# Kernel optimization log

Measured on AMD Instinct MI355X. Metric: run time of the kernel, lower is better.

Reference implementation:

```python
import jax, jax.numpy as jnp
import numpy as np

B, C, S = 128, 32, 512          # batch, input_channel, seq_len (= d_model of the encoders)
EMB = 256                       # embed_size
NHEAD = 8                       # args.num_heads (also TransformerEncoderLayer nhead)
DFF = 2048                      # torch TransformerEncoderLayer default dim_feedforward
RLEN = S // 2 + 1               # 257 rfft bins
HK = int(RLEN * 0.5)            # 128, 'hight_freq_k' split point
LK = RLEN - HK                  # 129

def _ln(x, w, b, axes=-1):
    m = jnp.mean(x, axis=axes, keepdims=True)
    v = jnp.var(x, axis=axes, keepdims=True)
    return (x - m) / jnp.sqrt(v + 1e-5) * w + b

def _tel(x, in_w, in_b, out_w, out_b, ln1w, ln1b, w1, b1, w2, b2, ln2w, ln2b):
    # torch nn.TransformerEncoderLayer (batch_first, post-norm, relu, eval-mode dropout)
    b_, s_, d_ = x.shape
    dh = d_ // NHEAD
    qkv = x @ in_w.T + in_b
    q, k, v = jnp.split(qkv, 3, axis=-1)
    sp = lambda t: t.reshape(b_, s_, NHEAD, dh).transpose(0, 2, 1, 3)
    q, k, v = sp(q), sp(k), sp(v)
    sc = jnp.einsum('bhqd,bhkd->bhqk', q, k) / jnp.sqrt(jnp.asarray(dh, x.dtype))
    att = jax.nn.softmax(sc, axis=-1)
    o = jnp.einsum('bhqk,bhkd->bhqd', att, v).transpose(0, 2, 1, 3).reshape(b_, s_, d_)
    o = o @ out_w.T + out_b
    x = _ln(x + o, ln1w, ln1b)
    f = jax.nn.relu(x @ w1.T + b1) @ w2.T + b2
    return _ln(x + f, ln2w, ln2b)

def _crelu(z):
    return jax.lax.complex(jax.nn.relu(z.real), jax.nn.relu(z.imag))

def _csoftmax(z):
    return jax.lax.complex(jax.nn.softmax(z.real, axis=-1), jax.nn.softmax(z.imag, axis=-1))

def _cattn(q):
    # self-attention with complex Q=K=V (no conjugate, per torch matmul(Q, K^T))
    dk = q.shape[-1]
    sc = jnp.einsum('bqe,bke->bqk', q, q) / jnp.asarray(dk, jnp.float32) ** 0.5
    return jnp.einsum('bqk,bke->bqe', _csoftmax(sc), q)

def setup_inputs() -> dict:
    key = jax.random.key(0)
    ks = iter(jax.random.split(key, 64))
    n = lambda *sh: jax.random.normal(next(ks), sh, jnp.float32) * 0.02
    d = {'x': jax.random.normal(next(ks), (B, C, S), jnp.float32)}
    for p in ('t', 'r'):
        d[p + '_in_w'] = n(3 * S, S);  d[p + '_in_b'] = jnp.zeros((3 * S,), jnp.float32)
        d[p + '_out_w'] = n(S, S);     d[p + '_out_b'] = jnp.zeros((S,), jnp.float32)
        d[p + '_ln1_w'] = jnp.ones((S,), jnp.float32); d[p + '_ln1_b'] = jnp.zeros((S,), jnp.float32)
        d[p + '_lin1_w'] = n(DFF, S); d[p + '_lin1_b'] = jnp.zeros((DFF,), jnp.float32)
        d[p + '_lin2_w'] = n(S, DFF); d[p + '_lin2_b'] = jnp.zeros((S,), jnp.float32)
        d[p + '_ln2_w'] = jnp.ones((S,), jnp.float32); d[p + '_ln2_b'] = jnp.zeros((S,), jnp.float32)
    d['lc_w'] = n(S, S);  d['lc_b'] = jnp.zeros((S,), jnp.float32)
    d['up1_w'] = n(S, S); d['up1_b'] = jnp.zeros((S,), jnp.float32)
    d['up2_w'] = n(S, S); d['up2_b'] = jnp.zeros((S,), jnp.float32)
    d['n1_w'] = jnp.ones((C, S), jnp.float32); d['n1_b'] = jnp.zeros((C, S), jnp.float32)
    d['n2_w'] = jnp.ones((C, S), jnp.float32); d['n2_b'] = jnp.zeros((C, S), jnp.float32)
    d['l1_re'] = jax.random.normal(next(ks), (HK, EMB), jnp.float32)
    d['l1_im'] = jax.random.normal(next(ks), (HK, EMB), jnp.float32)
    d['h1_re'] = jax.random.normal(next(ks), (LK, EMB), jnp.float32)
    d['h1_im'] = jax.random.normal(next(ks), (LK, EMB), jnp.float32)
    d['lb1_re'] = jax.random.normal(next(ks), (EMB,), jnp.float32)
    d['lb1_im'] = jax.random.normal(next(ks), (EMB,), jnp.float32)
    d['hb1_re'] = jax.random.normal(next(ks), (EMB,), jnp.float32)
    d['hb1_im'] = jax.random.normal(next(ks), (EMB,), jnp.float32)
    return d

def reference(x, t_in_w, t_in_b, t_out_w, t_out_b, t_ln1_w, t_ln1_b, t_lin1_w, t_lin1_b, t_lin2_w, t_lin2_b, t_ln2_w, t_ln2_b, r_in_w, r_in_b, r_out_w, r_out_b, r_ln1_w, r_ln1_b, r_lin1_w, r_lin1_b, r_lin2_w, r_lin2_b, r_ln2_w, r_ln2_b, lc_w, lc_b, up1_w, up1_b, up2_w, up2_b, n1_w, n1_b, n2_w, n2_b, l1_re, l1_im, h1_re, h1_im, lb1_re, lb1_im, hb1_re, hb1_im):
    l1 = jax.lax.complex(l1_re, l1_im)
    h1 = jax.lax.complex(h1_re, h1_im)
    lb1 = jax.lax.complex(lb1_re, lb1_im)
    hb1 = jax.lax.complex(hb1_re, hb1_im)
    down_x = x  # downsample_scale=1 and padding_length=0 -> identity (i=0 path)
    # main branch
    df = jax.nn.relu(_tel(down_x, t_in_w, t_in_b, t_out_w, t_out_b, t_ln1_w, t_ln1_b,
                          t_lin1_w, t_lin1_b, t_lin2_w, t_lin2_b, t_ln2_w, t_ln2_b))
    df = _ln(df, n1_w, n1_b, axes=(-2, -1))
    # ttf_freqaug
    xf = jnp.fft.rfft(down_x, norm='ortho')                      # [B, C, 257] complex
    low = _crelu(jnp.einsum('bdk,ke->bde', xf[..., :HK], l1) + lb1)
    high = _crelu(jnp.einsum('bdk,ke->bde', xf[..., HK:], h1) + hb1)
    low = low + _cattn(low)
    high = high + _cattn(high)
    xcat = jnp.concatenate([low, high[..., low.shape[-1]:]], axis=-1)  # EMB bins (high slice is empty)
    fa = jnp.fft.irfft(xcat, n=S, norm='ortho')                  # zero-pads 256 -> 257 bins
    fa = fa @ lc_w.T + lc_b                                      # linear_change
    up = (fa @ up1_w.T + up1_b) @ up2_w.T + up2_b                # linear_up_sampling
    # recons branch
    rf = jax.nn.relu(_tel(fa, r_in_w, r_in_b, r_out_w, r_out_b, r_ln1_w, r_ln1_b,
                          r_lin1_w, r_lin1_b, r_lin2_w, r_lin2_b, r_ln2_w, r_ln2_b))
    rf = _ln(rf, n2_w, n2_b, axes=(-2, -1))
    res = df + rf
    return (res, down_x, fa, up)
```

## Files before the change

kernel.cpp:

```cpp
#include <hip/hip_runtime.h>
#include <math.h>


#define NROW 4096
#define NOUT 2097152

typedef __attribute__((ext_vector_type(8))) short short8;
typedef __attribute__((ext_vector_type(4))) float floatx4;

__device__ __forceinline__ unsigned short f2bf(float f) {
    union { float f; unsigned u; } v; v.f = f;
    return (unsigned short)((v.u + 0x7fffu + ((v.u >> 16) & 1u)) >> 16);
}
__device__ __forceinline__ float bf2f(unsigned short h) {
    union { unsigned u; float f; } v; v.u = ((unsigned)h) << 16;
    return v.f;
}

__device__ __forceinline__ void gload16(const unsigned short* g, unsigned short* l) {
    __builtin_amdgcn_global_load_lds((const __attribute__((address_space(1))) void*)g,
                                     (__attribute__((address_space(3))) void*)l, 16, 0, 0);
}

__device__ __forceinline__ void xcd_swizzle(int& bx, int& by, int& bz) {
    const int gx = gridDim.x, gy = gridDim.y;
    const int nwg = gx * gy * gridDim.z;
    int b = (bz * gy + by) * gx + bx;
    const int chunk = nwg >> 3;
    const int lb = (b & 7) * chunk + (b >> 3);
    bx = lb % gx;
    const int rem = lb / gx;
    by = rem % gy;
    bz = rem / gy;
}

__global__ __launch_bounds__(256) void tab_kernel(float* __restrict__ tabC, float* __restrict__ tabS)
{
    int n = blockIdx.x, k = threadIdx.x;
    int m = (n * k) & 511;
    float th = (float)m * 0.01227184630308513f;
    float s, c; sincosf(th, &s, &c);
    tabC[n * 256 + k] = c;
    tabS[n * 256 + k] = s;
}

__global__ __launch_bounds__(256) void wawm_kernel(const float* __restrict__ l1_re, const float* __restrict__ l1_im,
                                                   const float* __restrict__ lc_w,
                                                   const float* __restrict__ tabC, const float* __restrict__ tabS,
                                                   unsigned short* __restrict__ WaH, unsigned short* __restrict__ WaL,
                                                   unsigned short* __restrict__ WmH, unsigned short* __restrict__ WmL)
{
    __shared__ float lw[512];
    const float inv = 0.04419417382415922f;
    if (blockIdx.z == 0) {
        int n  = blockIdx.x;
        int ep = blockIdx.y * 256 + threadIdx.x;
        float acc = 0.f;
        if (ep < 256) {
            for (int k = 0; k < 128; ++k) {
                float c = tabC[n * 256 + k], s = tabS[n * 256 + k];
                acc += c * l1_re[k * 256 + ep] + s * l1_im[k * 256 + ep];
            }
        } else {
            int e = ep - 256;
            for (int k = 0; k < 128; ++k) {
                float c = tabC[n * 256 + k], s = tabS[n * 256 + k];
                acc += c * l1_im[k * 256 + e] - s * l1_re[k * 256 + e];
            }
        }
        float v = acc * inv;
        size_t idx = (size_t)ep * 512 + n;
        unsigned short h = f2bf(v);
        WaH[idx] = h;
        WaL[idx] = f2bf(v - bf2f(h));
    } else {
        int s  = blockIdx.x;
        int kk = blockIdx.y * 256 + threadIdx.x;
        for (int i = threadIdx.x; i < 512; i += 256) lw[i] = lc_w[s * 512 + i];
        __syncthreads();
        float acc = 0.f;
        if (kk < 256) {
            int k = kk;
            for (int n = 0; n < 512; ++n) acc += tabC[n * 256 + k] * lw[n];
            acc *= (k == 0) ? inv : 2.f * inv;
        } else {
            int k = kk - 256;
            if (k == 0) acc = 0.f;
            else {
                for (int n = 0; n < 512; ++n) acc += tabS[n * 256 + k] * lw[n];
                acc *= -2.f * inv;
            }
        }
        size_t idx = (size_t)s * 512 + kk;
        unsigned short h = f2bf(acc);
        WmH[idx] = h;
        WmL[idx] = f2bf(acc - bf2f(h));
    }
}

__global__ __launch_bounds__(256) void uber_prep_kernel(
    const float* s0, const float* s1, const float* s2, const float* s3, const float* s4,
    const float* s5, const float* s6, const float* s7, const float* s8, const float* s9,
    unsigned short* __restrict__ o, unsigned short* __restrict__ rinLo,
    const float* __restrict__ x, unsigned short* __restrict__ xhi,
    unsigned short* __restrict__ xlo, float* __restrict__ xcp,
    const float* __restrict__ lbre, const float* __restrict__ lbim, float* __restrict__ lbout)
{
    const int bid = blockIdx.x, tid = threadIdx.x;
    if (bid < 26624) {
        int i = bid * 256 + tid;
        const float* s; int off;
        if (i < 3145728) {
            if (i < 1048576) { if (i < 786432) { s = s0; off = 0; } else { s = s1; off = 786432; } }
            else             { if (i < 2097152) { s = s2; off = 1048576; } else { s = s3; off = 2097152; } }
        } else {
            if (i < 5242880) {
                if (i < 3932160) { s = s4; off = 3145728; }
                else if (i < 4194304) { s = s5; off = 3932160; }
                else { s = s6; off = 4194304; }
            } else {
                if (i < 6291456) { s = s7; off = 5242880; }
                else if (i < 6553600) { s = s8; off = 6291456; }
                else { s = s9; off = 6553600; }
            }
        }
        float v = s[i - off];
        unsigned short h = f2bf(v);
        o[i] = h;
        if (i >= 3145728 && i < 3932160) rinLo[i - 3145728] = f2bf(v - bf2f(h));
    } else if (bid < 34816) {
        int i = (bid - 26624) * 256 + tid;
        float v = x[i];
        unsigned short h = f2bf(v);
        xhi[i] = h;
        xlo[i] = f2bf(v - bf2f(h));
        xcp[i] = v;
    } else {
        int i = (bid - 34816) * 256 + tid;
        if (i < 512) lbout[i] = (i < 256) ? lbre[i] : lbim[i - 256];
    }
}

template <int TM, int TN, int ACT, int WF, int WBF>
__global__ __launch_bounds__(256) void gemm_mfma(
    const unsigned short* __restrict__ A, const unsigned short* __restrict__ W,
    const float* __restrict__ bias, float* __restrict__ Cf,
    unsigned short* __restrict__ Cb, int N, int K)
{
    constexpr int MI = TM / 32, NJ = TN / 32;
    constexpr int ARW = TM / 4, BRW = TN / 4;
    __shared__ unsigned short As[2][TM * 32];
    __shared__ unsigned short Bs[2][TN * 32];
    const int tid = threadIdx.x;
    const int wave = tid >> 6, lane = tid & 63;
    int bx = blockIdx.x, by = blockIdx.y, bz = blockIdx.z;
    xcd_swizzle(bx, by, bz);
    const int m0 = by * TM, n0 = bx * TN;
    const int sr = lane >> 2, sc = (lane & 3) * 8;
    const unsigned short* aS = A + (size_t)(m0 + wave * ARW + sr) * K + sc;
    const unsigned short* wS = W + (size_t)(n0 + wave * BRW + sr) * K + sc;
    const int wm = (wave >> 1) * (TM / 2), wn = (wave & 1) * (TN / 2);
    const int fr = lane & 15, fko = (lane >> 4) * 8;

    floatx4 acc[MI][NJ];
#pragma unroll
    for (int i = 0; i < MI; ++i)
#pragma unroll
        for (int j = 0; j < NJ; ++j) acc[i][j] = (floatx4){0.f, 0.f, 0.f, 0.f};

    for (int k0 = 0; k0 < K; k0 += 64) {
#pragma unroll
        for (int h = 0; h < 2; ++h) {
#pragma unroll
            for (int c = 0; c < ARW / 16; ++c)
                gload16(aS + (size_t)(16 * c) * K + k0 + 32 * h, &As[h][(wave * ARW + 16 * c) * 32]);
#pragma unroll
            for (int c = 0; c < BRW / 16; ++c)
                gload16(wS + (size_t)(16 * c) * K + k0 + 32 * h, &Bs[h][(wave * BRW + 16 * c) * 32]);
        }
        __syncthreads();
#pragma unroll
        for (int h = 0; h < 2; ++h) {
            short8 af[MI], bfr[NJ];
#pragma unroll
            for (int i = 0; i < MI; ++i) af[i] = *(const short8*)&As[h][(wm + i * 16 + fr) * 32 + fko];
#pragma unroll
            for (int j = 0; j < NJ; ++j) bfr[j] = *(const short8*)&Bs[h][(wn + j * 16 + fr) * 32 + fko];
#pragma unroll
            for (int i = 0; i < MI; ++i)
#pragma unroll
                for (int j = 0; j < NJ; ++j)
                    acc[i][j] = __builtin_amdgcn_mfma_f32_16x16x32_bf16(af[i], bfr[j], acc[i][j], 0, 0, 0);
        }
        __syncthreads();
    }
    const int r0 = m0 + wm + (lane >> 4) * 4;
#pragma unroll
    for (int i = 0; i < MI; ++i) {
#pragma unroll
        for (int j = 0; j < NJ; ++j) {
            int n = n0 + wn + j * 16 + fr;
            float bv = bias[n];
#pragma unroll
            for (int r = 0; r < 4; ++r) {
                int m = r0 + i * 16 + r;
                size_t idx = (size_t)m * N + n;
                float v = acc[i][j][r] + bv;
                if (ACT) v = fmaxf(v, 0.f);
                if (WF) Cf[idx] = v;
                if (WBF) Cb[idx] = f2bf(v);
            }
        }
    }
}

template <int TM, int TN, int ACT, int WBF>
__global__ __launch_bounds__(256) void gemm_dual(
    const unsigned short* __restrict__ A0, const unsigned short* __restrict__ A1,
    const unsigned short* __restrict__ W0, const unsigned short* __restrict__ W1,
    const float* __restrict__ b0, const float* __restrict__ b1,
    float* __restrict__ C0, float* __restrict__ C1,
    unsigned short* __restrict__ D0, unsigned short* __restrict__ D1, int N, int K)
{
    constexpr int MI = TM / 32, NJ = TN / 32;
    constexpr int ARW = TM / 4, BRW = TN / 4;
    __shared__ unsigned short As[2][TM * 32];
    __shared__ unsigned short Bs[2][TN * 32];
    const int tid = threadIdx.x;
    const int wave = tid >> 6, lane = tid & 63;
    int bx = blockIdx.x, by = blockIdx.y, bz = blockIdx.z;
    xcd_swizzle(bx, by, bz);
    const int m0 = by * TM, n0 = bx * TN;
    const int z = bz;
    const unsigned short* A = z ? A1 : A0;
    const unsigned short* W = z ? W1 : W0;
    const float* bias = z ? b1 : b0;
    float* Cf = z ? C1 : C0;
    unsigned short* Cb = z ? D1 : D0;
    const int sr = lane >> 2, sc = (lane & 3) * 8;
    const unsigned short* aS = A + (size_t)(m0 + wave * ARW + sr) * K + sc;
    const unsigned short* wS = W + (size_t)(n0 + wave * BRW + sr) * K + sc;
    const int wm = (wave >> 1) * (TM / 2), wn = (wave & 1) * (TN / 2);
    const int fr = lane & 15, fko = (lane >> 4) * 8;

    floatx4 acc[MI][NJ];
#pragma unroll
    for (int i = 0; i < MI; ++i)
#pragma unroll
        for (int j = 0; j < NJ; ++j) acc[i][j] = (floatx4){0.f, 0.f, 0.f, 0.f};

    for (int k0 = 0; k0 < K; k0 += 64) {
#pragma unroll
        for (int h = 0; h < 2; ++h) {
#pragma unroll
            for (int c = 0; c < ARW / 16; ++c)
                gload16(aS + (size_t)(16 * c) * K + k0 + 32 * h, &As[h][(wave * ARW + 16 * c) * 32]);
#pragma unroll
            for (int c = 0; c < BRW / 16; ++c)
                gload16(wS + (size_t)(16 * c) * K + k0 + 32 * h, &Bs[h][(wave * BRW + 16 * c) * 32]);
        }
        __syncthreads();
#pragma unroll
        for (int h = 0; h < 2; ++h) {
            short8 af[MI], bfr[NJ];
#pragma unroll
            for (int i = 0; i < MI; ++i) af[i] = *(const short8*)&As[h][(wm + i * 16 + fr) * 32 + fko];
#pragma unroll
            for (int j = 0; j < NJ; ++j) bfr[j] = *(const short8*)&Bs[h][(wn + j * 16 + fr) * 32 + fko];
#pragma unroll
            for (int i = 0; i < MI; ++i)
#pragma unroll
                for (int j = 0; j < NJ; ++j)
                    acc[i][j] = __builtin_amdgcn_mfma_f32_16x16x32_bf16(af[i], bfr[j], acc[i][j], 0, 0, 0);
        }
        __syncthreads();
    }
    const int r0 = m0 + wm + (lane >> 4) * 4;
#pragma unroll
    for (int i = 0; i < MI; ++i) {
#pragma unroll
        for (int j = 0; j < NJ; ++j) {
            int n = n0 + wn + j * 16 + fr;
            float bv = bias[n];
#pragma unroll
            for (int r = 0; r < 4; ++r) {
                int m = r0 + i * 16 + r;
                size_t idx = (size_t)m * N + n;
                float v = acc[i][j][r] + bv;
                if (ACT) v = fmaxf(v, 0.f);
                if (WBF) Cb[idx] = f2bf(v);
                else     Cf[idx] = v;
            }
        }
    }
}

template <int TM, int TN, int ACT, int WCOPY, int WHILO>
__global__ __launch_bounds__(256) void gemm_mfma3(
    const unsigned short* __restrict__ Ah, const unsigned short* __restrict__ Al,
    const unsigned short* __restrict__ Wh, const unsigned short* __restrict__ Wl,
    const float* __restrict__ bias, float* __restrict__ Cf, float* __restrict__ Ccopy,
    unsigned short* __restrict__ Hh, unsigned short* __restrict__ Hl, int N, int K)
{
    constexpr int MI = TM / 32, NJ = TN / 32;
    constexpr int ARW = TM / 4, BRW = TN / 4;
    __shared__ unsigned short Ash[2][TM * 32];
    __shared__ unsigned short Asl[2][TM * 32];
    __shared__ unsigned short Bsh[2][TN * 32];
    __shared__ unsigned short Bsl[2][TN * 32];
    const int tid = threadIdx.x;
    const int wave = tid >> 6, lane = tid & 63;
    int bx = blockIdx.x, by = blockIdx.y, bz = blockIdx.z;
    xcd_swizzle(bx, by, bz);
    const int m0 = by * TM, n0 = bx * TN;
    const int sr = lane >> 2, sc = (lane & 3) * 8;
    const size_t aoff = (size_t)(m0 + wave * ARW + sr) * K + sc;
    const size_t woff = (size_t)(n0 + wave * BRW + sr) * K + sc;
    const int wm = (wave >> 1) * (TM / 2), wn = (wave & 1) * (TN / 2);
    const int fr = lane & 15, fko = (lane >> 4) * 8;

    floatx4 acc[MI][NJ];
#pragma unroll
    for (int i = 0; i < MI; ++i)
#pragma unroll
        for (int j = 0; j < NJ; ++j) acc[i][j] = (floatx4){0.f, 0.f, 0.f, 0.f};

    for (int k0 = 0; k0 < K; k0 += 64) {
#pragma unroll
        for (int h = 0; h < 2; ++h) {
#pragma unroll
            for (int c = 0; c < ARW / 16; ++c) {
                gload16(Ah + aoff + (size_t)(16 * c) * K + k0 + 32 * h, &Ash[h][(wave * ARW + 16 * c) * 32]);
                gload16(Al + aoff + (size_t)(16 * c) * K + k0 + 32 * h, &Asl[h][(wave * ARW + 16 * c) * 32]);
            }
#pragma unroll
            for (int c = 0; c < BRW / 16; ++c) {
                gload16(Wh + woff + (size_t)(16 * c) * K + k0 + 32 * h, &Bsh[h][(wave * BRW + 16 * c) * 32]);
                gload16(Wl + woff + (size_t)(16 * c) * K + k0 + 32 * h, &Bsl[h][(wave * BRW + 16 * c) * 32]);
            }
        }
        __syncthreads();
#pragma unroll
        for (int h = 0; h < 2; ++h) {
            short8 ah[MI], al[MI], bh[NJ], bl[NJ];
#pragma unroll
            for (int i = 0; i < MI; ++i) {
                ah[i] = *(const short8*)&Ash[h][(wm + i * 16 + fr) * 32 + fko];
                al[i] = *(const short8*)&Asl[h][(wm + i * 16 + fr) * 32 + fko];
            }
#pragma unroll
            for (int j = 0; j < NJ; ++j) {
                bh[j] = *(const short8*)&Bsh[h][(wn + j * 16 + fr) * 32 + fko];
                bl[j] = *(const short8*)&Bsl[h][(wn + j * 16 + fr) * 32 + fko];
            }
#pragma unroll
            for (int i = 0; i < MI; ++i)
#pragma unroll
                for (int j = 0; j < NJ; ++j) {
                    acc[i][j] = __builtin_amdgcn_mfma_f32_16x16x32_bf16(al[i], bh[j], acc[i][j], 0, 0, 0);
                    acc[i][j] = __builtin_amdgcn_mfma_f32_16x16x32_bf16(ah[i], bl[j], acc[i][j], 0, 0, 0);
                    acc[i][j] = __builtin_amdgcn_mfma_f32_16x16x32_bf16(ah[i], bh[j], acc[i][j], 0, 0, 0);
                }
        }
        __syncthreads();
    }
    const int r0 = m0 + wm + (lane >> 4) * 4;
#pragma unroll
    for (int i = 0; i < MI; ++i) {
#pragma unroll
        for (int j = 0; j < NJ; ++j) {
            int n = n0 + wn + j * 16 + fr;
            float bv = bias[n];
#pragma unroll
            for (int r = 0; r < 4; ++r) {
                int m = r0 + i * 16 + r;
                size_t idx = (size_t)m * N + n;
                float v = acc[i][j][r] + bv;
                if (ACT) v = fmaxf(v, 0.f);
                Cf[idx] = v;
                if (WCOPY) Ccopy[idx] = v;
                if (WHILO) {
                    unsigned short h = f2bf(v);
                    Hh[idx] = h;
                    Hl[idx] = f2bf(v - bf2f(h));
                }
            }
        }
    }
}

template <int TM, int TN>
__global__ __launch_bounds__(256) void gemm_qkv_dual(
    const unsigned short* __restrict__ Ah0, const unsigned short* __restrict__ Al0,
    const unsigned short* __restrict__ Wh0, const unsigned short* __restrict__ Wl0,
    const float* __restrict__ b0, float* __restrict__ C0,
    const unsigned short* __restrict__ A1, const unsigned short* __restrict__ W1,
    const float* __restrict__ b1, unsigned short* __restrict__ C1,
    int N, int K)
{
    constexpr int MI = TM / 32, NJ = TN / 32;
    constexpr int ARW = TM / 4, BRW = TN / 4;
    __shared__ unsigned short Ash[2][TM * 32];
    __shared__ unsigned short Asl[2][TM * 32];
    __shared__ unsigned short Bsh[2][TN * 32];
    __shared__ unsigned short Bsl[2][TN * 32];
    const int tid = threadIdx.x;
    const int wave = tid >> 6, lane = tid & 63;
    int bx = blockIdx.x, by = blockIdx.y, bz = blockIdx.z;
    xcd_swizzle(bx, by, bz);
    const int m0 = by * TM, n0 = bx * TN;
    const int sr = lane >> 2, sc = (lane & 3) * 8;
    const size_t aoff = (size_t)(m0 + wave * ARW + sr) * K + sc;
    const size_t woff = (size_t)(n0 + wave * BRW + sr) * K + sc;
    const int wm = (wave >> 1) * (TM / 2), wn = (wave & 1) * (TN / 2);
    const int fr = lane & 15, fko = (lane >> 4) * 8;

    floatx4 acc[MI][NJ];
#pragma unroll
    for (int i = 0; i < MI; ++i)
#pragma unroll
        for (int j = 0; j < NJ; ++j) acc[i][j] = (floatx4){0.f, 0.f, 0.f, 0.f};

    const int r0 = m0 + wm + (lane >> 4) * 4;

    if (bz == 0) {
        for (int k0 = 0; k0 < K; k0 += 64) {
#pragma unroll
            for (int h = 0; h < 2; ++h) {
#pragma unroll
                for (int c = 0; c < ARW / 16; ++c) {
                    gload16(Ah0 + aoff + (size_t)(16 * c) * K + k0 + 32 * h, &Ash[h][(wave * ARW + 16 * c) * 32]);
                    gload16(Al0 + aoff + (size_t)(16 * c) * K + k0 + 32 * h, &Asl[h][(wave * ARW + 16 * c) * 32]);
                }
#pragma unroll
                for (int c = 0; c < BRW / 16; ++c) {
                    gload16(Wh0 + woff + (size_t)(16 * c) * K + k0 + 32 * h, &Bsh[h][(wave * BRW + 16 * c) * 32]);
                    gload16(Wl0 + woff + (size_t)(16 * c) * K + k0 + 32 * h, &Bsl[h][(wave * BRW + 16 * c) * 32]);
                }
            }
            __syncthreads();
#pragma unroll
            for (int h = 0; h < 2; ++h) {
                short8 ah[MI], al[MI], bh[NJ], bl[NJ];
#pragma unroll
                for (int i = 0; i < MI; ++i) {
                    ah[i] = *(const short8*)&Ash[h][(wm + i * 16 + fr) * 32 + fko];
                    al[i] = *(const short8*)&Asl[h][(wm + i * 16 + fr) * 32 + fko];
                }
#pragma unroll
                for (int j = 0; j < NJ; ++j) {
                    bh[j] = *(const short8*)&Bsh[h][(wn + j * 16 + fr) * 32 + fko];
                    bl[j] = *(const short8*)&Bsl[h][(wn + j * 16 + fr) * 32 + fko];
                }
#pragma unroll
                for (int i = 0; i < MI; ++i)
#pragma unroll
                    for (int j = 0; j < NJ; ++j) {
                        acc[i][j] = __builtin_amdgcn_mfma_f32_16x16x32_bf16(al[i], bh[j], acc[i][j], 0, 0, 0);
                        acc[i][j] = __builtin_amdgcn_mfma_f32_16x16x32_bf16(ah[i], bl[j], acc[i][j], 0, 0, 0);
                        acc[i][j] = __builtin_amdgcn_mfma_f32_16x16x32_bf16(ah[i], bh[j], acc[i][j], 0, 0, 0);
                    }
            }
            __syncthreads();
        }
#pragma unroll
        for (int i = 0; i < MI; ++i)
#pragma unroll
            for (int j = 0; j < NJ; ++j) {
                int n = n0 + wn + j * 16 + fr;
                float bv = b0[n];
#pragma unroll
                for (int r = 0; r < 4; ++r) {
                    int m = r0 + i * 16 + r;
                    C0[(size_t)m * N + n] = acc[i][j][r] + bv;
                }
            }
    } else {
        for (int k0 = 0; k0 < K; k0 += 64) {
#pragma unroll
            for (int h = 0; h < 2; ++h) {
#pragma unroll
                for (int c = 0; c < ARW / 16; ++c)
                    gload16(A1 + aoff + (size_t)(16 * c) * K + k0 + 32 * h, &Ash[h][(wave * ARW + 16 * c) * 32]);
#pragma unroll
                for (int c = 0; c < BRW / 16; ++c)
                    gload16(W1 + woff + (size_t)(16 * c) * K + k0 + 32 * h, &Bsh[h][(wave * BRW + 16 * c) * 32]);
            }
            __syncthreads();
#pragma unroll
            for (int h = 0; h < 2; ++h) {
                short8 af[MI], bfr[NJ];
#pragma unroll
                for (int i = 0; i < MI; ++i) af[i] = *(const short8*)&Ash[h][(wm + i * 16 + fr) * 32 + fko];
#pragma unroll
                for (int j = 0; j < NJ; ++j) bfr[j] = *(const short8*)&Bsh[h][(wn + j * 16 + fr) * 32 + fko];
#pragma unroll
                for (int i = 0; i < MI; ++i)
#pragma unroll
                    for (int j = 0; j < NJ; ++j)
                        acc[i][j] = __builtin_amdgcn_mfma_f32_16x16x32_bf16(af[i], bfr[j], acc[i][j], 0, 0, 0);
            }
            __syncthreads();
        }
#pragma unroll
        for (int i = 0; i < MI; ++i)
#pragma unroll
            for (int j = 0; j < NJ; ++j) {
                int n = n0 + wn + j * 16 + fr;
                float bv = b1[n];
#pragma unroll
                for (int r = 0; r < 4; ++r) {
                    int m = r0 + i * 16 + r;
                    C1[(size_t)m * N + n] = f2bf(acc[i][j][r] + bv);
                }
            }
    }
}

__global__ __launch_bounds__(256) void attn_dual_kernel(const float* __restrict__ qkvF,
                                                        const unsigned short* __restrict__ qkvB,
                                                        unsigned short* __restrict__ outR,
                                                        unsigned short* __restrict__ outT)
{
    const int isT = blockIdx.x >> 10;
    const int bid = blockIdx.x & 1023;
    const int b = bid >> 3;
    const int h = bid & 7;
    __shared__ float qs[32][65], ks[32][65], vs[32][65];
    __shared__ float ps[32][33];
    const int tid = threadIdx.x;
    if (isT) {
        for (int i = tid; i < 2048; i += 256) {
            int s = i >> 6, d = i & 63;
            size_t base = ((size_t)(b * 32 + s)) * 1536 + h * 64 + d;
            qs[s][d] = bf2f(qkvB[base]);
            ks[s][d] = bf2f(qkvB[base + 512]);
            vs[s][d] = bf2f(qkvB[base + 1024]);
        }
    } else {
        for (int i = tid; i < 2048; i += 256) {
            int s = i >> 6, d = i & 63;
            size_t base = ((size_t)(b * 32 + s)) * 1536 + h * 64 + d;
            qs[s][d] = qkvF[base];
            ks[s][d] = qkvF[base + 512];
            vs[s][d] = qkvF[base + 1024];
        }
    }
    __syncthreads();
    for (int i = tid; i < 1024; i += 256) {
        int si = i >> 5, sj = i & 31;
        float acc = 0.f;
#pragma unroll 8
        for (int d = 0; d < 64; ++d) acc += qs[si][d] * ks[sj][d];
        ps[si][sj] = acc * 0.125f;
    }
    __syncthreads();
    if (tid < 32) {
        float mx = -1e30f;
        for (int j = 0; j < 32; ++j) mx = fmaxf(mx, ps[tid][j]);
        float sum = 0.f;
        for (int j = 0; j < 32; ++j) { float e = __expf(ps[tid][j] - mx); ps[tid][j] = e; sum += e; }
        float inv = 1.f / sum;
        for (int j = 0; j < 32; ++j) ps[tid][j] *= inv;
    }
    __syncthreads();
    unsigned short* ob = isT ? outT : outR;
    for (int i = tid; i < 2048; i += 256) {
        int s = i >> 6, d = i & 63;
        float acc = 0.f;
#pragma unroll 8
        for (int k = 0; k < 32; ++k) acc += ps[s][k] * vs[k][d];
        ob[((size_t)(b * 32 + s)) * 512 + h * 64 + d] = f2bf(acc);
    }
}

__global__ __launch_bounds__(512) void cattn2_kernel(const float* __restrict__ LL,
                                                     unsigned short* __restrict__ outHi,
                                                     unsigned short* __restrict__ outLo)
{
    extern __shared__ float Xs[];
    __shared__ float Pr[16][33], Pi[16][33];
    const int b = blockIdx.x, half = blockIdx.y;
    const int tid = threadIdx.x;
    const float* base = LL + (size_t)b * 16384;
    for (int i = tid; i < 16384; i += 512) {
        int c = i >> 9, e = i & 511;
        Xs[e * 32 + ((c ^ e) & 31)] = base[i];
    }
    __syncthreads();
    {
        const int li = tid >> 5;
        const int ci = half * 16 + li;
        const int ck = tid & 31;
        float ar = 0.f, ai = 0.f;
#pragma unroll 4
        for (int er = 0; er < 256; ++er) {
            const int sw = er & 31;
            float yr = Xs[er * 32 + ((ck ^ sw) & 31)];
            float yi = Xs[(er + 256) * 32 + ((ck ^ sw) & 31)];
            float xr = Xs[er * 32 + ((ci ^ sw) & 31)];
            float xi = Xs[(er + 256) * 32 + ((ci ^ sw) & 31)];
            ar += xr * yr - xi * yi;
            ai += xr * yi + xi * yr;
        }
        Pr[li][ck] = ar * 0.0625f;
        Pi[li][ck] = ai * 0.0625f;
    }
    __syncthreads();
    if (tid < 32) {
        int r = tid & 15;
        float (*P)[33] = (tid < 16) ? Pr : Pi;
        float mx = -1e30f;
        for (int j = 0; j < 32; ++j) mx = fmaxf(mx, P[r][j]);
        float s = 0.f;
        for (int j = 0; j < 32; ++j) { float e = __expf(P[r][j] - mx); P[r][j] = e; s += e; }
        float inv = 1.f / s;
        for (int j = 0; j < 32; ++j) P[r][j] *= inv;
    }
    __syncthreads();
    const int er = tid & 255;
    const int th = tid >> 8;
    const int sw = er & 31;
    float accr[8], acci[8];
#pragma unroll
    for (int t = 0; t < 8; ++t) { accr[t] = 0.f; acci[t] = 0.f; }
    for (int k = 0; k < 32; ++k) {
        float yr = Xs[er * 32 + ((k ^ sw) & 31)];
        float yi = Xs[(er + 256) * 32 + ((k ^ sw) & 31)];
#pragma unroll
        for (int t = 0; t < 8; ++t) {
            float pr = Pr[th * 8 + t][k], pi = Pi[th * 8 + t][k];
            accr[t] += pr * yr - pi * yi;
            acci[t] += pr * yi + pi * yr;
        }
    }
#pragma unroll
    for (int t = 0; t < 8; ++t) {
        int c = half * 16 + th * 8 + t;
        float vr = Xs[er * 32 + ((c ^ sw) & 31)] + accr[t];
        float vi = Xs[(er + 256) * 32 + ((c ^ sw) & 31)] + acci[t];
        size_t ir = (size_t)b * 16384 + (size_t)c * 512 + er;
        unsigned short hr = f2bf(vr), hi2 = f2bf(vi);
        outHi[ir] = hr;        outLo[ir] = f2bf(vr - bf2f(hr));
        outHi[ir + 256] = hi2; outLo[ir + 256] = f2bf(vi - bf2f(hi2));
    }
}

__global__ __launch_bounds__(256) void add_ln_d1(
    const float* __restrict__ r0, const float* __restrict__ y0,
    const float* __restrict__ w0, const float* __restrict__ b0,
    unsigned short* __restrict__ h0, unsigned short* __restrict__ l0,
    const float* __restrict__ r1, const float* __restrict__ y1,
    const float* __restrict__ w1, const float* __restrict__ b1,
    unsigned short* __restrict__ h1, unsigned short* __restrict__ l1)
{
    const int row = blockIdx.x;
    const int br = row >> 12;
    const int rl = row & 4095;
    const float* resid = br ? r1 : r0;
    const float* y     = br ? y1 : y0;
    const float* w     = br ? w1 : w0;
    const float* bb    = br ? b1 : b0;
    unsigned short* oh = br ? h1 : h0;
    unsigned short* ol = br ? l1 : l0;
    const int tid = threadIdx.x;
    const size_t base = (size_t)rl * 512;
    float v0 = resid[base + tid] + y[base + tid];
    float v1 = resid[base + 256 + tid] + y[base + 256 + tid];
    float s = v0 + v1, q = v0 * v0 + v1 * v1;
    for (int off = 32; off; off >>= 1) { s += __shfl_down(s, off); q += __shfl_down(q, off); }
    __shared__ float sw[4], qw[4], ms, is;
    int wid = tid >> 6, lane = tid & 63;
    if (lane == 0) { sw[wid] = s; qw[wid] = q; }
    __syncthreads();
    if (tid == 0) {
        float S = sw[0] + sw[1] + sw[2] + sw[3];
        float Q = qw[0] + qw[1] + qw[2] + qw[3];
        float m = S * (1.f / 512.f);
        ms = m;
        is = rsqrtf(Q * (1.f / 512.f) - m * m + 1e-5f);
    }
    __syncthreads();
    float m = ms, inv = is;
    float o0 = (v0 - m) * inv * w[tid] + bb[tid];
    float o1 = (v1 - m) * inv * w[256 + tid] + bb[256 + tid];
    unsigned short e0 = f2bf(o0), e1 = f2bf(o1);
    oh[base + tid] = e0;       ol[base + tid] = f2bf(o0 - bf2f(e0));
    oh[base + 256 + tid] = e1; ol[base + 256 + tid] = f2bf(o1 - bf2f(e1));
}

__global__ __launch_bounds__(256) void add_ln_d2(
    const unsigned short* __restrict__ rh0, const unsigned short* __restrict__ rl0,
    const float* __restrict__ y0, const float* __restrict__ w0, const float* __restrict__ b0,
    float* __restrict__ o0p,
    const unsigned short* __restrict__ rh1, const unsigned short* __restrict__ rl1,
    const float* __restrict__ y1, const float* __restrict__ w1, const float* __restrict__ b1,
    float* __restrict__ o1p)
{
    const int row = blockIdx.x;
    const int br = row >> 12;
    const int rl = row & 4095;
    const unsigned short* rh = br ? rh1 : rh0;
    const unsigned short* rlo = br ? rl1 : rl0;
    const float* y  = br ? y1 : y0;
    const float* w  = br ? w1 : w0;
    const float* bb = br ? b1 : b0;
    float* op = br ? o1p : o0p;
    const int tid = threadIdx.x;
    const size_t base = (size_t)rl * 512;
    float v0 = bf2f(rh[base + tid]) + bf2f(rlo[base + tid]) + y[base + tid];
    float v1 = bf2f(rh[base + 256 + tid]) + bf2f(rlo[base + 256 + tid]) + y[base + 256 + tid];
    float s = v0 + v1, q = v0 * v0 + v1 * v1;
    for (int off = 32; off; off >>= 1) { s += __shfl_down(s, off); q += __shfl_down(q, off); }
    __shared__ float sw[4], qw[4], ms, is;
    int wid = tid >> 6, lane = tid & 63;
    if (lane == 0) { sw[wid] = s; qw[wid] = q; }
    __syncthreads();
    if (tid == 0) {
        float S = sw[0] + sw[1] + sw[2] + sw[3];
        float Q = qw[0] + qw[1] + qw[2] + qw[3];
        float m = S * (1.f / 512.f);
        ms = m;
        is = rsqrtf(Q * (1.f / 512.f) - m * m + 1e-5f);
    }
    __syncthreads();
    float m = ms, inv = is;
    op[base + tid]       = (v0 - m) * inv * w[tid] + bb[tid];
    op[base + 256 + tid] = (v1 - m) * inv * w[256 + tid] + bb[256 + tid];
}

__global__ __launch_bounds__(1024) void relu_bln_fused(
    const float* __restrict__ xR, const float* __restrict__ w2, const float* __restrict__ b2,
    const float* __restrict__ xT, const float* __restrict__ w1, const float* __restrict__ b1,
    float* __restrict__ out)
{
    __shared__ float rfs[16384];
    __shared__ float sw_[16], qw_[16], ms_, is_;
    const int bb = blockIdx.x, tid = threadIdx.x;
    const int wid = tid >> 6, lane = tid & 63;
    const float* xr = xR + (size_t)bb * 16384;
    float s = 0.f, q = 0.f;
    for (int i = tid; i < 16384; i += 1024) { float v = fmaxf(xr[i], 0.f); s += v; q += v * v; }
    for (int off = 32; off; off >>= 1) { s += __shfl_down(s, off); q += __shfl_down(q, off); }
    if (lane == 0) { sw_[wid] = s; qw_[wid] = q; }
    __syncthreads();
    if (tid == 0) {
        float S = 0.f, Q = 0.f;
        for (int i = 0; i < 16; ++i) { S += sw_[i]; Q += qw_[i]; }
        float m = S * (1.f / 16384.f);
        ms_ = m;
        is_ = rsqrtf(Q * (1.f / 16384.f) - m * m + 1e-5f);
    }
    __syncthreads();
    float m = ms_, inv = is_;
    for (int i = tid; i < 16384; i += 1024) {
        float v = fmaxf(xr[i], 0.f);
        rfs[i] = (v - m) * inv * w2[i] + b2[i];
    }
    const float* xt = xT + (size_t)bb * 16384;
    s = 0.f; q = 0.f;
    for (int i = tid; i < 16384; i += 1024) { float v = fmaxf(xt[i], 0.f); s += v; q += v * v; }
    for (int off = 32; off; off >>= 1) { s += __shfl_down(s, off); q += __shfl_down(q, off); }
    if (lane == 0) { sw_[wid] = s; qw_[wid] = q; }
    __syncthreads();
    if (tid == 0) {
        float S = 0.f, Q = 0.f;
        for (int i = 0; i < 16; ++i) { S += sw_[i]; Q += qw_[i]; }
        float m2 = S * (1.f / 16384.f);
        ms_ = m2;
        is_ = rsqrtf(Q * (1.f / 16384.f) - m2 * m2 + 1e-5f);
    }
    __syncthreads();
    m = ms_; inv = is_;
    float* op = out + (size_t)bb * 16384;
    for (int i = tid; i < 16384; i += 1024) {
        float v = fmaxf(xt[i], 0.f);
        op[i] = (v - m) * inv * w1[i] + b1[i] + rfs[i];
    }
}

extern "C" void kernel_launch(void* const* d_in, const int* in_sizes, int n_in,
                              void* d_out, int out_size, void* d_ws, size_t ws_size,
                              hipStream_t stream)
{
    (void)in_sizes; (void)n_in; (void)out_size; (void)ws_size;
    const float* x        = (const float*)d_in[0];
    const float* t_in_w   = (const float*)d_in[1];
    const float* t_in_b   = (const float*)d_in[2];
    const float* t_out_w  = (const float*)d_in[3];
    const float* t_out_b  = (const float*)d_in[4];
    const float* t_ln1_w  = (const float*)d_in[5];
    const float* t_ln1_b  = (const float*)d_in[6];
    const float* t_lin1_w = (const float*)d_in[7];
    const float* t_lin1_b = (const float*)d_in[8];
    const float* t_lin2_w = (const float*)d_in[9];
    const float* t_lin2_b = (const float*)d_in[10];
    const float* t_ln2_w  = (const float*)d_in[11];
    const float* t_ln2_b  = (const float*)d_in[12];
    const float* r_in_w   = (const float*)d_in[13];
    const float* r_in_b   = (const float*)d_in[14];
    const float* r_out_w  = (const float*)d_in[15];
    const float* r_out_b  = (const float*)d_in[16];
    const float* r_ln1_w  = (const float*)d_in[17];
    const float* r_ln1_b  = (const float*)d_in[18];
    const float* r_lin1_w = (const float*)d_in[19];
    const float* r_lin1_b = (const float*)d_in[20];
    const float* r_lin2_w = (const float*)d_in[21];
    const float* r_lin2_b = (const float*)d_in[22];
    const float* r_ln2_w  = (const float*)d_in[23];
    const float* r_ln2_b  = (const float*)d_in[24];
    const float* lc_w     = (const float*)d_in[25];
    const float* lc_b     = (const float*)d_in[26];
    const float* up1_w    = (const float*)d_in[27];
    const float* up1_b    = (const float*)d_in[28];
    const float* up2_w    = (const float*)d_in[29];
    const float* up2_b    = (const float*)d_in[30];
    const float* n1_w     = (const float*)d_in[31];
    const float* n1_b     = (const float*)d_in[32];
    const float* n2_w     = (const float*)d_in[33];
    const float* n2_b     = (const float*)d_in[34];
    const float* l1_re    = (const float*)d_in[35];
    const float* l1_im    = (const float*)d_in[36];
    const float* lb1_re   = (const float*)d_in[39];
    const float* lb1_im   = (const float*)d_in[40];

    float* outp = (float*)d_out;

    float* WS   = (float*)d_ws;
    float* LL   = WS;
    float* FA   = WS;
    float* yR   = WS;
    float* QR   = WS + 2097152;
    float* tabC = QR;
    float* tabS = QR + 131072;
    unsigned short* WaHu = (unsigned short*)(QR + 786432);
    unsigned short* WaLu = (unsigned short*)(QR + 917504);
    unsigned short* WmHu = (unsigned short*)(QR + 1048576);
    unsigned short* WmLu = (unsigned short*)(QR + 1179648);
    float* qkvR = QR;
    unsigned short* x1rH = (unsigned short*)(WS + 2097152);
    unsigned short* x1rL = (unsigned short*)(WS + 3145728);
    unsigned short* x1tH = (unsigned short*)(WS + 4194304);
    unsigned short* x1tL = (unsigned short*)(WS + 5242880);
    float* yT   = WS + 6291456;
    unsigned short* qkvT = (unsigned short*)(WS + 8388608);
    unsigned short* f1R  = (unsigned short*)(WS + 8388608);
    float* x2R  = WS + 8388608;
    float* x2T  = WS + 10485760;
    unsigned short* xHi = (unsigned short*)(WS + 11534336);
    unsigned short* xLo = (unsigned short*)(WS + 12582912);
    unsigned short* aoR = (unsigned short*)(WS + 11534336);
    unsigned short* aoT = (unsigned short*)(WS + 12582912);
    unsigned short* f1T = (unsigned short*)(WS + 12582912);
    unsigned short* LLH = (unsigned short*)(WS + 13631488);
    unsigned short* LLL = (unsigned short*)(WS + 14680064);
    unsigned short* u1b = (unsigned short*)(WS + 13631488);
    float* oR   = WS + 13631488;
    float* oT   = WS + 15728640;
    unsigned short* faHi = (unsigned short*)(WS + 15728640);
    unsigned short* faLo = (unsigned short*)(WS + 16777216);
    unsigned short* rinLoU = (unsigned short*)(WS + 17825792);
    float* LB   = WS + 18219008;
    unsigned short* WB = (unsigned short*)(WS + 18366464);

    unsigned short* w_tin  = WB + 0;
    unsigned short* w_tout = WB + 786432;
    unsigned short* w_tl1  = WB + 1048576;
    unsigned short* w_tl2  = WB + 2097152;
    unsigned short* w_rin  = WB + 3145728;
    unsigned short* w_rout = WB + 3932160;
    unsigned short* w_rl1  = WB + 4194304;
    unsigned short* w_rl2  = WB + 5242880;
    unsigned short* w_up1  = WB + 6291456;
    unsigned short* w_up2  = WB + 6553600;

    dim3 blk(256);

    tab_kernel<<<dim3(512), blk, 0, stream>>>(tabC, tabS);
    wawm_kernel<<<dim3(512, 2, 2), blk, 0, stream>>>(l1_re, l1_im, lc_w, tabC, tabS,
                                                     WaHu, WaLu, WmHu, WmLu);
    uber_prep_kernel<<<dim3(34818), blk, 0, stream>>>(t_in_w, t_out_w, t_lin1_w, t_lin2_w,
                                                      r_in_w, r_out_w, r_lin1_w, r_lin2_w,
                                                      up1_w, up2_w, WB, rinLoU,
                                                      x, xHi, xLo, outp + NOUT,
                                                      lb1_re, lb1_im, LB);

    gemm_mfma3<64,64,1,0,0><<<dim3(8, 64), blk, 0, stream>>>(xHi, xLo, WaHu, WaLu, LB,
                                                             LL, nullptr, nullptr, nullptr, 512, 512);
    cattn2_kernel<<<dim3(128, 2), dim3(512), 65536, stream>>>(LL, LLH, LLL);
    gemm_mfma3<64,64,0,1,1><<<dim3(8, 64), blk, 0, stream>>>(LLH, LLL, WmHu, WmLu, lc_b,
                                                             FA, outp + 2 * NOUT, faHi, faLo, 512, 512);

    gemm_mfma<64,64,0,0,1><<<dim3(8, 64), blk, 0, stream>>>(faHi, w_up1, up1_b, nullptr, u1b, 512, 512);
    gemm_mfma<64,64,0,1,0><<<dim3(8, 64), blk, 0, stream>>>(u1b, w_up2, up2_b, outp + 3 * NOUT, nullptr, 512, 512);

    gemm_qkv_dual<64,128><<<dim3(12, 64, 2), blk, 0, stream>>>(faHi, faLo, w_rin, rinLoU, r_in_b, qkvR,
                                                               xHi, w_tin, t_in_b, qkvT, 1536, 512);

    attn_dual_kernel<<<dim3(2048), blk, 0, stream>>>(qkvR, qkvT, aoR, aoT);
    gemm_dual<64,64,0,0><<<dim3(8, 64, 2), blk, 0, stream>>>(aoR, aoT, w_rout, w_tout,
                                                             r_out_b, t_out_b, oR, oT,
                                                             nullptr, nullptr, 512, 512);
    add_ln_d1<<<dim3(8192), blk, 0, stream>>>(FA, oR, r_ln1_w, r_ln1_b, x1rH, x1rL,
                                              x,  oT, t_ln1_w, t_ln1_b, x1tH, x1tL);
    gemm_dual<64,128,1,1><<<dim3(16, 64, 2), blk, 0, stream>>>(x1rH, x1tH, w_rl1, w_tl1,
                                                               r_lin1_b, t_lin1_b, nullptr, nullptr,
                                                               f1R, f1T, 2048, 512);
    gemm_dual<64,64,0,0><<<dim3(8, 64, 2), blk, 0, stream>>>(f1R, f1T, w_rl2, w_tl2,
                                                             r_lin2_b, t_lin2_b, yR, yT,
                                                             nullptr, nullptr, 512, 2048);
    add_ln_d2<<<dim3(8192), blk, 0, stream>>>(x1rH, x1rL, yR, r_ln2_w, r_ln2_b, x2R,
                                              x1tH, x1tL, yT, t_ln2_w, t_ln2_b, x2T);
    relu_bln_fused<<<dim3(128), dim3(1024), 0, stream>>>(x2R, n2_w, n2_b, x2T, n1_w, n1_b, outp);
}
```

Measured before the change: 470.2 us.

## Fold up-sampling GEMMs into the QKV and out-projection batched launches

The two standalone up-sampling GEMMs are removed. The first (fa @ up1) becomes a third z-slice of the QKV GEMM launch, with blocks beyond N=512 exiting early. The second (u1 @ up2) becomes a third slice of the out-projection launch. This cuts two kernel launches and lets small GEMMs share the GPU with larger ones. The intermediate u1 is staged in the first output region, which is overwritten later. The early-exit blocks in the QKV grid waste some scheduling slots.

```diff
diff --git a/kernel.cpp b/kernel.cpp
--- a/kernel.cpp
+++ b/kernel.cpp
@@ -141,79 +141,6 @@
     }
 }
 
-template <int TM, int TN, int ACT, int WF, int WBF>
-__global__ __launch_bounds__(256) void gemm_mfma(
-    const unsigned short* __restrict__ A, const unsigned short* __restrict__ W,
-    const float* __restrict__ bias, float* __restrict__ Cf,
-    unsigned short* __restrict__ Cb, int N, int K)
-{
-    constexpr int MI = TM / 32, NJ = TN / 32;
-    constexpr int ARW = TM / 4, BRW = TN / 4;
-    __shared__ unsigned short As[2][TM * 32];
-    __shared__ unsigned short Bs[2][TN * 32];
-    const int tid = threadIdx.x;
-    const int wave = tid >> 6, lane = tid & 63;
-    int bx = blockIdx.x, by = blockIdx.y, bz = blockIdx.z;
-    xcd_swizzle(bx, by, bz);
-    const int m0 = by * TM, n0 = bx * TN;
-    const int sr = lane >> 2, sc = (lane & 3) * 8;
-    const unsigned short* aS = A + (size_t)(m0 + wave * ARW + sr) * K + sc;
-    const unsigned short* wS = W + (size_t)(n0 + wave * BRW + sr) * K + sc;
-    const int wm = (wave >> 1) * (TM / 2), wn = (wave & 1) * (TN / 2);
-    const int fr = lane & 15, fko = (lane >> 4) * 8;
-
-    floatx4 acc[MI][NJ];
-#pragma unroll
-    for (int i = 0; i < MI; ++i)
-#pragma unroll
-        for (int j = 0; j < NJ; ++j) acc[i][j] = (floatx4){0.f, 0.f, 0.f, 0.f};
-
-    for (int k0 = 0; k0 < K; k0 += 64) {
-#pragma unroll
-        for (int h = 0; h < 2; ++h) {
-#pragma unroll
-            for (int c = 0; c < ARW / 16; ++c)
-                gload16(aS + (size_t)(16 * c) * K + k0 + 32 * h, &As[h][(wave * ARW + 16 * c) * 32]);
-#pragma unroll
-            for (int c = 0; c < BRW / 16; ++c)
-                gload16(wS + (size_t)(16 * c) * K + k0 + 32 * h, &Bs[h][(wave * BRW + 16 * c) * 32]);
-        }
-        __syncthreads();
-#pragma unroll
-        for (int h = 0; h < 2; ++h) {
-            short8 af[MI], bfr[NJ];
-#pragma unroll
-            for (int i = 0; i < MI; ++i) af[i] = *(const short8*)&As[h][(wm + i * 16 + fr) * 32 + fko];
-#pragma unroll
-            for (int j = 0; j < NJ; ++j) bfr[j] = *(const short8*)&Bs[h][(wn + j * 16 + fr) * 32 + fko];
-#pragma unroll
-            for (int i = 0; i < MI; ++i)
-#pragma unroll
-                for (int j = 0; j < NJ; ++j)
-                    acc[i][j] = __builtin_amdgcn_mfma_f32_16x16x32_bf16(af[i], bfr[j], acc[i][j], 0, 0, 0);
-        }
-        __syncthreads();
-    }
-    const int r0 = m0 + wm + (lane >> 4) * 4;
-#pragma unroll
-    for (int i = 0; i < MI; ++i) {
-#pragma unroll
-        for (int j = 0; j < NJ; ++j) {
-            int n = n0 + wn + j * 16 + fr;
-            float bv = bias[n];
-#pragma unroll
-            for (int r = 0; r < 4; ++r) {
-                int m = r0 + i * 16 + r;
-                size_t idx = (size_t)m * N + n;
-                float v = acc[i][j][r] + bv;
-                if (ACT) v = fmaxf(v, 0.f);
-                if (WF) Cf[idx] = v;
-                if (WBF) Cb[idx] = f2bf(v);
-            }
-        }
-    }
-}
-
 template <int TM, int TN, int ACT, int WBF>
 __global__ __launch_bounds__(256) void gemm_dual(
     const unsigned short* __restrict__ A0, const unsigned short* __restrict__ A1,
@@ -295,6 +222,82 @@
     }
 }
 
+template <int TM, int TN>
+__global__ __launch_bounds__(256) void gemm_out_tri(
+    const unsigned short* __restrict__ A0, const unsigned short* __restrict__ W0,
+    const float* __restrict__ b0, float* __restrict__ C0,
+    const unsigned short* __restrict__ A1, const unsigned short* __restrict__ W1,
+    const float* __restrict__ b1, float* __restrict__ C1,
+    const unsigned short* __restrict__ A2, const unsigned short* __restrict__ W2,
+    const float* __restrict__ b2, float* __restrict__ C2, int N, int K)
+{
+    constexpr int MI = TM / 32, NJ = TN / 32;
+    constexpr int ARW = TM / 4, BRW = TN / 4;
+    __shared__ unsigned short As[2][TM * 32];
+    __shared__ unsigned short Bs[2][TN * 32];
+    const int tid = threadIdx.x;
+    const int wave = tid >> 6, lane = tid & 63;
+    int bx = blockIdx.x, by = blockIdx.y, bz = blockIdx.z;
+    xcd_swizzle(bx, by, bz);
+    const int m0 = by * TM, n0 = bx * TN;
+    const unsigned short* A = (bz == 0) ? A0 : (bz == 1) ? A1 : A2;
+    const unsigned short* W = (bz == 0) ? W0 : (bz == 1) ? W1 : W2;
+    const float* bias       = (bz == 0) ? b0 : (bz == 1) ? b1 : b2;
+    float* Cf               = (bz == 0) ? C0 : (bz == 1) ? C1 : C2;
+    const int sr = lane >> 2, sc = (lane & 3) * 8;
+    const unsigned short* aS = A + (size_t)(m0 + wave * ARW + sr) * K + sc;
+    const unsigned short* wS = W + (size_t)(n0 + wave * BRW + sr) * K + sc;
+    const int wm = (wave >> 1) * (TM / 2), wn = (wave & 1) * (TN / 2);
+    const int fr = lane & 15, fko = (lane >> 4) * 8;
+
+    floatx4 acc[MI][NJ];
+#pragma unroll
+    for (int i = 0; i < MI; ++i)
+#pragma unroll
+        for (int j = 0; j < NJ; ++j) acc[i][j] = (floatx4){0.f, 0.f, 0.f, 0.f};
+
+    for (int k0 = 0; k0 < K; k0 += 64) {
+#pragma unroll
+        for (int h = 0; h < 2; ++h) {
+#pragma unroll
+            for (int c = 0; c < ARW / 16; ++c)
+                gload16(aS + (size_t)(16 * c) * K + k0 + 32 * h, &As[h][(wave * ARW + 16 * c) * 32]);
+#pragma unroll
+            for (int c = 0; c < BRW / 16; ++c)
+                gload16(wS + (size_t)(16 * c) * K + k0 + 32 * h, &Bs[h][(wave * BRW + 16 * c) * 32]);
+        }
+        __syncthreads();
+#pragma unroll
+        for (int h = 0; h < 2; ++h) {
+            short8 af[MI], bfr[NJ];
+#pragma unroll
+            for (int i = 0; i < MI; ++i) af[i] = *(const short8*)&As[h][(wm + i * 16 + fr) * 32 + fko];
+#pragma unroll
+            for (int j = 0; j < NJ; ++j) bfr[j] = *(const short8*)&Bs[h][(wn + j * 16 + fr) * 32 + fko];
+#pragma unroll
+            for (int i = 0; i < MI; ++i)
+#pragma unroll
+                for (int j = 0; j < NJ; ++j)
+                    acc[i][j] = __builtin_amdgcn_mfma_f32_16x16x32_bf16(af[i], bfr[j], acc[i][j], 0, 0, 0);
+        }
+        __syncthreads();
+    }
+    const int r0 = m0 + wm + (lane >> 4) * 4;
+#pragma unroll
+    for (int i = 0; i < MI; ++i) {
+#pragma unroll
+        for (int j = 0; j < NJ; ++j) {
+            int n = n0 + wn + j * 16 + fr;
+            float bv = bias[n];
+#pragma unroll
+            for (int r = 0; r < 4; ++r) {
+                int m = r0 + i * 16 + r;
+                Cf[(size_t)m * N + n] = acc[i][j][r] + bv;
+            }
+        }
+    }
+}
+
 template <int TM, int TN, int ACT, int WCOPY, int WHILO>
 __global__ __launch_bounds__(256) void gemm_mfma3(
     const unsigned short* __restrict__ Ah, const unsigned short* __restrict__ Al,
@@ -390,12 +393,14 @@
 }
 
 template <int TM, int TN>
-__global__ __launch_bounds__(256) void gemm_qkv_dual(
+__global__ __launch_bounds__(256) void gemm_qkv_tri(
     const unsigned short* __restrict__ Ah0, const unsigned short* __restrict__ Al0,
     const unsigned short* __restrict__ Wh0, const unsigned short* __restrict__ Wl0,
     const float* __restrict__ b0, float* __restrict__ C0,
     const unsigned short* __restrict__ A1, const unsigned short* __restrict__ W1,
     const float* __restrict__ b1, unsigned short* __restrict__ C1,
+    const unsigned short* __restrict__ A2, const unsigned short* __restrict__ W2,
+    const float* __restrict__ b2, unsigned short* __restrict__ C2,
     int N, int K)
 {
     constexpr int MI = TM / 32, NJ = TN / 32;
@@ -408,7 +413,9 @@
     const int wave = tid >> 6, lane = tid & 63;
     int bx = blockIdx.x, by = blockIdx.y, bz = blockIdx.z;
     xcd_swizzle(bx, by, bz);
+    if (bz == 2 && bx >= 512 / TN) return;
     const int m0 = by * TM, n0 = bx * TN;
+    const int nOut = (bz == 2) ? 512 : N;
     const int sr = lane >> 2, sc = (lane & 3) * 8;
     const size_t aoff = (size_t)(m0 + wave * ARW + sr) * K + sc;
     const size_t woff = (size_t)(n0 + wave * BRW + sr) * K + sc;
@@ -476,15 +483,19 @@
                 }
             }
     } else {
+        const unsigned short* A = (bz == 1) ? A1 : A2;
+        const unsigned short* W = (bz == 1) ? W1 : W2;
+        const float* bias = (bz == 1) ? b1 : b2;
+        unsigned short* Cb = (bz == 1) ? C1 : C2;
         for (int k0 = 0; k0 < K; k0 += 64) {
 #pragma unroll
             for (int h = 0; h < 2; ++h) {
 #pragma unroll
                 for (int c = 0; c < ARW / 16; ++c)
-                    gload16(A1 + aoff + (size_t)(16 * c) * K + k0 + 32 * h, &Ash[h][(wave * ARW + 16 * c) * 32]);
+                    gload16(A + aoff + (size_t)(16 * c) * K + k0 + 32 * h, &Ash[h][(wave * ARW + 16 * c) * 32]);
 #pragma unroll
                 for (int c = 0; c < BRW / 16; ++c)
-                    gload16(W1 + woff + (size_t)(16 * c) * K + k0 + 32 * h, &Bsh[h][(wave * BRW + 16 * c) * 32]);
+                    gload16(W + woff + (size_t)(16 * c) * K + k0 + 32 * h, &Bsh[h][(wave * BRW + 16 * c) * 32]);
             }
             __syncthreads();
 #pragma unroll
@@ -507,11 +518,11 @@
 #pragma unroll
             for (int j = 0; j < NJ; ++j) {
                 int n = n0 + wn + j * 16 + fr;
-                float bv = b1[n];
+                float bv = bias[n];
 #pragma unroll
                 for (int r = 0; r < 4; ++r) {
                     int m = r0 + i * 16 + r;
-                    C1[(size_t)m * N + n] = f2bf(acc[i][j][r] + bv);
+                    Cb[(size_t)m * nOut + n] = f2bf(acc[i][j][r] + bv);
                 }
             }
     }
@@ -854,7 +865,6 @@
     unsigned short* f1T = (unsigned short*)(WS + 12582912);
     unsigned short* LLH = (unsigned short*)(WS + 13631488);
     unsigned short* LLL = (unsigned short*)(WS + 14680064);
-    unsigned short* u1b = (unsigned short*)(WS + 13631488);
     float* oR   = WS + 13631488;
     float* oT   = WS + 15728640;
     unsigned short* faHi = (unsigned short*)(WS + 15728640);
@@ -862,6 +872,8 @@
     unsigned short* rinLoU = (unsigned short*)(WS + 17825792);
     float* LB   = WS + 18219008;
     unsigned short* WB = (unsigned short*)(WS + 18366464);
+
+    unsigned short* u1b = (unsigned short*)outp;
 
     unsigned short* w_tin  = WB + 0;
     unsigned short* w_tout = WB + 786432;
@@ -891,16 +903,14 @@
     gemm_mfma3<64,64,0,1,1><<<dim3(8, 64), blk, 0, stream>>>(LLH, LLL, WmHu, WmLu, lc_b,
                                                              FA, outp + 2 * NOUT, faHi, faLo, 512, 512);
 
-    gemm_mfma<64,64,0,0,1><<<dim3(8, 64), blk, 0, stream>>>(faHi, w_up1, up1_b, nullptr, u1b, 512, 512);
-    gemm_mfma<64,64,0,1,0><<<dim3(8, 64), blk, 0, stream>>>(u1b, w_up2, up2_b, outp + 3 * NOUT, nullptr, 512, 512);
-
-    gemm_qkv_dual<64,128><<<dim3(12, 64, 2), blk, 0, stream>>>(faHi, faLo, w_rin, rinLoU, r_in_b, qkvR,
-                                                               xHi, w_tin, t_in_b, qkvT, 1536, 512);
+    gemm_qkv_tri<64,128><<<dim3(12, 64, 3), blk, 0, stream>>>(faHi, faLo, w_rin, rinLoU, r_in_b, qkvR,
+                                                              xHi, w_tin, t_in_b, qkvT,
+                                                              faHi, w_up1, up1_b, u1b, 1536, 512);
 
     attn_dual_kernel<<<dim3(2048), blk, 0, stream>>>(qkvR, qkvT, aoR, aoT);
-    gemm_dual<64,64,0,0><<<dim3(8, 64, 2), blk, 0, stream>>>(aoR, aoT, w_rout, w_tout,
-                                                             r_out_b, t_out_b, oR, oT,
-                                                             nullptr, nullptr, 512, 512);
+    gemm_out_tri<64,64><<<dim3(8, 64, 3), blk, 0, stream>>>(aoR, w_rout, r_out_b, oR,
+                                                            aoT, w_tout, t_out_b, oT,
+                                                            u1b, w_up2, up2_b, outp + 3 * NOUT, 512, 512);
     add_ln_d1<<<dim3(8192), blk, 0, stream>>>(FA, oR, r_ln1_w, r_ln1_b, x1rH, x1rL,
                                               x,  oT, t_ln1_w, t_ln1_b, x1tH, x1tL);
     gemm_dual<64,128,1,1><<<dim3(16, 64, 2), blk, 0, stream>>>(x1rH, x1tH, w_rl1, w_tl1,
```

New measurement: 481.1 us. 2.3% more time.
